# Kernel tuning notes

Hardware: AMD Instinct MI355X
Metric: run time of the kernel (lower is better)

## Reference

```python
import jax, jax.numpy as jnp
import numpy as np

S, B, E, H = 2048, 4, 512, 8
HD = E // H


def setup_inputs() -> dict:
    key = jax.random.key(0)
    ks = jax.random.split(key, 5)
    scale = 1.0 / np.sqrt(E)
    return {
        "query": jax.random.normal(ks[0], (S, B, E), jnp.float32),
        "key": jax.random.normal(ks[1], (S, B, E), jnp.float32),
        "value": jax.random.normal(ks[2], (S, B, E), jnp.float32),
        "in_proj_weight": jax.random.normal(ks[3], (3 * E, E), jnp.float32) * scale,
        "in_proj_bias": jnp.zeros((3 * E,), jnp.float32),
        "out_proj_weight": jax.random.normal(ks[4], (E, E), jnp.float32) * scale,
        "out_proj_bias": jnp.zeros((E,), jnp.float32),
    }


def reference(query, key, value, in_proj_weight, in_proj_bias, out_proj_weight, out_proj_bias):
    tgt_len, bsz, embed_dim = query.shape
    src_len = key.shape[0]
    # Quirk of this module: first chunk (w_qk) projects BOTH q and k; third chunk projects v.
    w_qk = in_proj_weight[:embed_dim]
    w_v = in_proj_weight[2 * embed_dim:]
    b_qk = in_proj_bias[:embed_dim]
    b_v = in_proj_bias[2 * embed_dim:]
    q = query @ w_qk.T + b_qk          # [S, B, E]
    k = key @ w_qk.T + b_qk
    v = value @ w_v.T + b_v
    # (S, B, E) -> (B*H, S, HD)
    def split_heads(x, n):
        return x.reshape(n, bsz * H, HD).transpose(1, 0, 2)
    q = split_heads(q, tgt_len) / jnp.sqrt(jnp.asarray(HD, q.dtype))
    k = split_heads(k, src_len)
    v = split_heads(v, src_len)
    scores = jnp.einsum("bqd,bkd->bqk", q, k)          # [B*H, S, S] full score matrix
    attn = jax.nn.softmax(scores, axis=-1)
    out = jnp.einsum("bqk,bkd->bqd", attn, v)          # [B*H, S, HD]
    out = out.transpose(1, 0, 2).reshape(tgt_len * bsz, embed_dim)
    out = out @ out_proj_weight.T + out_proj_bias
    return out.reshape(tgt_len, bsz, embed_dim)
```

## Files before the change

### kernel.cpp

```cpp
#include <hip/hip_runtime.h>
#include <hip/hip_bf16.h>

typedef __attribute__((ext_vector_type(8))) short s16x8;
typedef __attribute__((ext_vector_type(4))) short s16x4;
typedef __attribute__((ext_vector_type(4))) float f32x4;

#if __has_builtin(__builtin_amdgcn_exp2f)
#define EXP2F(x) __builtin_amdgcn_exp2f(x)
#else
#define EXP2F(x) exp2f(x)
#endif

#define S_LEN 2048
#define EMB   512
#define MROWS 8192

__device__ __forceinline__ short f2bf(float f) {
    union { float f; unsigned u; } z; z.f = f;
    unsigned r = z.u + 0x7FFF + ((z.u >> 16) & 1);
    return (short)(r >> 16);
}
__device__ __forceinline__ short f2bf_fast(float f) {
    union { float f; unsigned u; } z; z.f = f;
    return (short)((z.u + 0x8000u) >> 16);
}
__device__ __forceinline__ int swzs(int s) { return s ^ ((s >> 3) & 7); }

__device__ __forceinline__ void barrier_fast() {
    asm volatile("s_waitcnt lgkmcnt(0)" ::: "memory");
    __builtin_amdgcn_s_barrier();
    __builtin_amdgcn_sched_barrier(0);
}

__global__ __launch_bounds__(256) void w_to_bf16(const float* __restrict__ W,
                                                 short* __restrict__ wb, int n)
{
    int i = (blockIdx.x * 256 + threadIdx.x) * 8;
    if (i < n) {
        f32x4 a = *(const f32x4*)(W + i);
        f32x4 b = *(const f32x4*)(W + i + 4);
        s16x8 o;
        o[0] = f2bf(a[0]); o[1] = f2bf(a[1]); o[2] = f2bf(a[2]); o[3] = f2bf(a[3]);
        o[4] = f2bf(b[0]); o[5] = f2bf(b[1]); o[6] = f2bf(b[2]); o[7] = f2bf(b[3]);
        *(s16x8*)(wb + i) = o;
    }
}

template<int AF32, int BF32>
__device__ __forceinline__ void gemm_mainloop(const void* __restrict__ Ag,
                                              const void* __restrict__ Bg,
                                              short* sA, short* sB,
                                              f32x4 acc[2][4], int K)
{
    const int tid  = threadIdx.x;
    const int lane = tid & 63;
    const int wv   = tid >> 6;
    const int lsw  = lane ^ ((lane >> 3) & 7);
    const int amt  = (wv >> 1) * 2;
    const int bnt  = (wv & 1) * 4;

    const int brow = tid >> 2, bqd = tid & 3;
    const int boff = swzs((brow >> 4) * 64 + bqd * 16 + (brow & 15)) * 8;
    const int frow = tid >> 3, ffc = tid & 7;
    const int foff = swzs((frow >> 4) * 64 + (ffc >> 1) * 16 + (frow & 15)) * 8
                   + (ffc & 1) * 4;

    f32x4 aF0[2], aF1[2], bF0[2], bF1[2];
    s16x8 aH0, aH1, bH0, bH1;

    auto loadA = [&](int kt, f32x4 fr[2], s16x8& hr) {
        if (AF32) {
            const float* g = (const float*)Ag + (size_t)frow * K + kt + ffc * 4;
            fr[0] = *(const f32x4*)g;
            fr[1] = *(const f32x4*)(g + (size_t)64 * K);
        } else {
            hr = *(const s16x8*)((const short*)Ag + (size_t)brow * K + kt + bqd * 8);
        }
    };
    auto loadB = [&](int kt, f32x4 fr[2], s16x8& hr) {
        if (BF32) {
            const float* g = (const float*)Bg + (size_t)frow * K + kt + ffc * 4;
            fr[0] = *(const f32x4*)g;
            fr[1] = *(const f32x4*)(g + (size_t)64 * K);
        } else {
            hr = *(const s16x8*)((const short*)Bg + (size_t)brow * K + kt + bqd * 8);
        }
    };
    auto commit = [&](short* s, f32x4 fr[2], s16x8& hr, int F32) {
        if (F32) {
#pragma unroll
            for (int p = 0; p < 2; ++p) {
                s16x4 o4;
                o4[0] = f2bf_fast(fr[p][0]); o4[1] = f2bf_fast(fr[p][1]);
                o4[2] = f2bf_fast(fr[p][2]); o4[3] = f2bf_fast(fr[p][3]);
                *(s16x4*)(s + foff + p * 2048) = o4;
            }
        } else {
            *(s16x8*)(s + boff) = hr;
        }
    };
    auto compute = [&](const short* sAc, const short* sBc) {
        s16x8 a[2], b[4];
#pragma unroll
        for (int i = 0; i < 2; ++i)
            a[i] = *(const s16x8*)(sAc + ((amt + i) * 64 + lsw) * 8);
#pragma unroll
        for (int j = 0; j < 4; ++j)
            b[j] = *(const s16x8*)(sBc + ((bnt + j) * 64 + lsw) * 8);
#pragma unroll
        for (int i = 0; i < 2; ++i)
#pragma unroll
            for (int j = 0; j < 4; ++j)
                acc[i][j] = __builtin_amdgcn_mfma_f32_16x16x32_bf16(a[i], b[j], acc[i][j], 0, 0, 0);
    };

    loadA(0, aF0, aH0);  loadB(0, bF0, bH0);
    loadA(32, aF1, aH1); loadB(32, bF1, bH1);
    commit(sA, aF0, aH0, AF32); commit(sB, bF0, bH0, BF32);
    barrier_fast();

    for (int kt = 0; kt < K; kt += 64) {
        const int k2 = (kt + 64 < K) ? kt + 64 : 0;
        loadA(k2, aF0, aH0); loadB(k2, bF0, bH0);
        compute(sA, sB);
        commit(sA + 4096, aF1, aH1, AF32); commit(sB + 4096, bF1, bH1, BF32);
        barrier_fast();
        const int k3 = (kt + 96 < K) ? kt + 96 : 0;
        loadA(k3, aF1, aH1); loadB(k3, bF1, bH1);
        compute(sA + 4096, sB + 4096);
        commit(sA, aF0, aH0, AF32); commit(sB, bF0, bH0, BF32);
        barrier_fast();
    }
}

__global__ __launch_bounds__(512, 4) void qkv_proj(const float* __restrict__ query,
                                                   const float* __restrict__ key,
                                                   const float* __restrict__ value,
                                                   const short* __restrict__ wb,
                                                   const float* __restrict__ bias,
                                                   short* __restrict__ q,
                                                   short* __restrict__ k,
                                                   short* __restrict__ vt)
{
    __shared__ __align__(16) short smem[16384];
    short* sA = smem;
    short* sB = smem + 8192;

    const int z = blockIdx.z;
    const float* X  = (z == 0) ? query : (z == 1) ? key : value;
    const short* Wz = wb   + (z == 2 ? (size_t)1024 * EMB : 0);
    const float* bz = bias + (z == 2 ? 1024 : 0);
    const float scale = (z == 0) ? 0.125f * 1.44269504f : 1.0f;

    const int blockM = blockIdx.x * 128, blockN = blockIdx.y * 128;

    f32x4 acc[2][4];
#pragma unroll
    for (int i = 0; i < 2; ++i)
#pragma unroll
        for (int j = 0; j < 4; ++j)
            acc[i][j] = (f32x4){0.f, 0.f, 0.f, 0.f};

    gemm_mainloop<1, 0>(X + (size_t)blockM * EMB, Wz + (size_t)blockN * EMB,
                        sA, sB, acc, EMB);

    const int tid = threadIdx.x, lane = tid & 63, wv = tid >> 6;
    const int l15 = lane & 15, quad = lane >> 4;
    const int wm = (wv >> 1) * 32, wn = (wv & 1) * 64;

#pragma unroll
    for (int j = 0; j < 4; ++j) {
        int colL = wn + j * 16 + l15;
        float bval = bz[blockN + colL];
        int hL = colL >> 6, hd = colL & 63;
#pragma unroll
        for (int i = 0; i < 2; ++i) {
#pragma unroll
            for (int r = 0; r < 4; ++r) {
                int rowL = wm + i * 16 + quad * 4 + r;
                int b = rowL & 3, sp = rowL >> 2;
                float val = (acc[i][j][r] + bval) * scale;
                int idx;
                if (z == 2) {
                    int R = (b * 2 + hL) * 64 + hd;
                    idx = R * 32 + (((sp >> 3) ^ (R & 3)) << 3) + (sp & 7);
                } else {
                    idx = ((b * 2 + hL) * 32 + sp) * 64 + hd;
                }
                smem[idx] = f2bf(val);
            }
        }
    }
    barrier_fast();

    if (z == 2) {
        int R = tid;
        int b = tid >> 7, hL = (tid >> 6) & 1, hd = tid & 63;
        int h = (blockN >> 6) + hL;
        short* dst = vt + ((size_t)(b * 8 + h) * 64 + hd) * 2048 + (blockM >> 2);
#pragma unroll
        for (int u = 0; u < 4; ++u)
            ((s16x8*)dst)[u] = *(const s16x8*)(smem + R * 32 + ((u ^ (R & 3)) << 3));
    } else {
        const s16x8* src = (const s16x8*)(smem + tid * 32);
        int b = tid >> 7, hL = (tid >> 6) & 1;
        int sp = (tid >> 1) & 31, hdh = (tid & 1) * 32;
        int h = (blockN >> 6) + hL;
        short* dstp = (z == 0) ? q : k;
        short* dst = dstp + ((size_t)(b * 8 + h) * 2048 + (blockM >> 2) + sp) * 64 + hdh;
#pragma unroll
        for (int u = 0; u < 4; ++u) ((s16x8*)dst)[u] = src[u];
    }
}

__global__ __launch_bounds__(256, 2) void flash_attn(const short* __restrict__ q,
                                                     const short* __restrict__ k,
                                                     const short* __restrict__ vt,
                                                     short* __restrict__ attn)
{
    __shared__ __align__(16) short sK[2][4096];
    __shared__ __align__(16) short sV[2][4096];
    const int bh = blockIdx.x;
    const int q0 = blockIdx.y * 128;
    const int tid = threadIdx.x, wv = tid >> 6, lane = tid & 63;
    const int l15 = lane & 15, quad = lane >> 4;
    const int lsw = lane ^ ((lane >> 3) & 7);

    s16x8 qf[2][2];
#pragma unroll
    for (int qr = 0; qr < 2; ++qr) {
        const short* qp = q + ((size_t)(bh * 2048 + q0 + wv * 32 + qr * 16 + l15)) * 64 + quad * 8;
        qf[qr][0] = *(const s16x8*)qp;
        qf[qr][1] = *(const s16x8*)(qp + 32);
    }

    const short* kg = k  + (size_t)bh * 2048 * 64;
    const short* vg = vt + (size_t)bh * 64 * 2048;

    const int rk = tid >> 2, qd = tid & 3;
    const int pr = (rk & 35) | ((rk & 24) >> 1) | ((rk & 4) << 2);
    const int kw0 = swzs((pr >> 4) * 64 + qd * 16 + (pr & 15)) * 8;
    const int vw0 = swzs((rk >> 4) * 64 + qd * 16 + (rk & 15)) * 8;
    const short* kgt = kg + (size_t)rk * 64 + qd * 8;
    const short* vgt = vg + (size_t)rk * 2048 + qd * 8;

    f32x4 o[2][4];
    float ls[2][4];
#pragma unroll
    for (int qr = 0; qr < 2; ++qr)
#pragma unroll
        for (int i = 0; i < 4; ++i) { o[qr][i] = (f32x4){0.f, 0.f, 0.f, 0.f}; ls[qr][i] = 0.f; }

    s16x8 ka0, kb0, va0, vb0, ka1, kb1, va1, vb1;
    auto loadF = [&](int kt, s16x8& ka, s16x8& kb, s16x8& va, s16x8& vb) {
        ka = *(const s16x8*)(kgt + (size_t)kt * 64);
        kb = *(const s16x8*)(kgt + (size_t)kt * 64 + 32);
        va = *(const s16x8*)(vgt + kt);
        vb = *(const s16x8*)(vgt + kt + 32);
    };
    auto commitF = [&](short* Kb, short* Vb, s16x8& ka, s16x8& kb, s16x8& va, s16x8& vb) {
        *(s16x8*)(Kb + kw0)        = ka;
        *(s16x8*)(Kb + kw0 + 2048) = kb;
        *(s16x8*)(Vb + vw0)        = va;
        *(s16x8*)(Vb + vw0 + 2048) = vb;
    };
    auto computeT = [&](const short* Kc, const short* Vc) {
        f32x4 sc[2][4];
#pragma unroll
        for (int ct = 0; ct < 4; ++ct) {
            s16x8 kf0 = *(const s16x8*)(Kc + (ct * 64 + lsw) * 8);
            s16x8 kf1 = *(const s16x8*)(Kc + (ct * 64 + lsw) * 8 + 2048);
#pragma unroll
            for (int qr = 0; qr < 2; ++qr) {
                f32x4 c = (f32x4){0.f, 0.f, 0.f, 0.f};
                c = __builtin_amdgcn_mfma_f32_16x16x32_bf16(kf0, qf[qr][0], c, 0, 0, 0);
                c = __builtin_amdgcn_mfma_f32_16x16x32_bf16(kf1, qf[qr][1], c, 0, 0, 0);
                sc[qr][ct] = c;
            }
        }
        s16x8 pf[2][2];
#pragma unroll
        for (int qr = 0; qr < 2; ++qr)
#pragma unroll
            for (int c = 0; c < 2; ++c)
#pragma unroll
                for (int h = 0; h < 2; ++h)
#pragma unroll
                    for (int r = 0; r < 4; ++r) {
                        float p = EXP2F(sc[qr][2 * c + h][r]);
                        ls[qr][r] += p;
                        pf[qr][c][h * 4 + r] = f2bf_fast(p);
                    }
#pragma unroll
        for (int nt = 0; nt < 4; ++nt)
#pragma unroll
            for (int c = 0; c < 2; ++c) {
                s16x8 vf = *(const s16x8*)(Vc + ((c * 4 + nt) * 64 + lsw) * 8);
#pragma unroll
                for (int qr = 0; qr < 2; ++qr)
                    o[qr][nt] = __builtin_amdgcn_mfma_f32_16x16x32_bf16(pf[qr][c], vf, o[qr][nt], 0, 0, 0);
            }
    };

    loadF(0, ka0, kb0, va0, vb0);
    loadF(64, ka1, kb1, va1, vb1);
    commitF(sK[0], sV[0], ka0, kb0, va0, vb0);
    barrier_fast();

    for (int kt = 0; kt < 2048; kt += 128) {
        loadF((kt + 128) & 2047, ka0, kb0, va0, vb0);
        computeT(sK[0], sV[0]);
        commitF(sK[1], sV[1], ka1, kb1, va1, vb1);
        barrier_fast();
        loadF((kt + 192) & 2047, ka1, kb1, va1, vb1);
        computeT(sK[1], sV[1]);
        commitF(sK[0], sV[0], ka0, kb0, va0, vb0);
        barrier_fast();
    }

    const int b = bh >> 3, h = bh & 7;
#pragma unroll
    for (int qr = 0; qr < 2; ++qr) {
        float s = ls[qr][0] + ls[qr][1] + ls[qr][2] + ls[qr][3];
        s += __shfl_xor(s, 16, 64);
        s += __shfl_xor(s, 32, 64);
        float sinv = 1.0f / s;
        float inv[4];
#pragma unroll
        for (int r = 0; r < 4; ++r)
            inv[r] = __shfl(sinv, quad * 20 + r, 64);
#pragma unroll
        for (int r = 0; r < 4; ++r) {
            int srow = q0 + wv * 32 + qr * 16 + quad * 4 + r;
#pragma unroll
            for (int nt = 0; nt < 4; ++nt)
                attn[(size_t)(srow * 4 + b) * 512 + h * 64 + nt * 16 + l15] = f2bf(o[qr][nt][r] * inv[r]);
        }
    }
}

__global__ __launch_bounds__(512, 4) void out_proj(const short* __restrict__ attn,
                                                   const float* __restrict__ W,
                                                   const float* __restrict__ bias,
                                                   float* __restrict__ out)
{
    __shared__ __align__(16) short sA[2 * 4096], sB[2 * 4096];
    const int blockM = blockIdx.x * 128, blockN = blockIdx.y * 128;

    f32x4 acc[2][4];
#pragma unroll
    for (int i = 0; i < 2; ++i)
#pragma unroll
        for (int j = 0; j < 4; ++j)
            acc[i][j] = (f32x4){0.f, 0.f, 0.f, 0.f};

    gemm_mainloop<0, 1>(attn + (size_t)blockM * EMB, W + (size_t)blockN * EMB,
                        sA, sB, acc, EMB);

    const int tid = threadIdx.x, lane = tid & 63, wv = tid >> 6;
    const int l15 = lane & 15, quad = lane >> 4;
    const int wm = (wv >> 1) * 32, wn = (wv & 1) * 64;

#pragma unroll
    for (int j = 0; j < 4; ++j) {
        int col = blockN + wn + j * 16 + l15;
        float bval = bias[col];
#pragma unroll
        for (int i = 0; i < 2; ++i) {
#pragma unroll
            for (int r = 0; r < 4; ++r) {
                int row = blockM + wm + i * 16 + quad * 4 + r;
                out[(size_t)row * 512 + col] = acc[i][j][r] + bval;
            }
        }
    }
}

extern "C" void kernel_launch(void* const* d_in, const int* in_sizes, int n_in,
                              void* d_out, int out_size, void* d_ws, size_t ws_size,
                              hipStream_t stream)
{
    const float* query = (const float*)d_in[0];
    const float* key   = (const float*)d_in[1];
    const float* value = (const float*)d_in[2];
    const float* ipw   = (const float*)d_in[3];
    const float* ipb   = (const float*)d_in[4];
    const float* opw   = (const float*)d_in[5];
    const float* opb   = (const float*)d_in[6];
    float* out = (float*)d_out;

    const size_t NELEM = (size_t)MROWS * EMB;
    short* q    = (short*)d_ws;
    short* k    = q + NELEM;
    short* attn = k + NELEM;
    short* vt   = (short*)d_out;
    short* wb   = (short*)d_out + NELEM;

    w_to_bf16 <<<dim3(384),      256, 0, stream>>>(ipw, wb, 1536 * EMB);
    qkv_proj  <<<dim3(64, 4, 3), 512, 0, stream>>>(query, key, value, wb, ipb, q, k, vt);
    flash_attn<<<dim3(32, 16),   256, 0, stream>>>(q, k, vt, attn);
    out_proj  <<<dim3(64, 4),    512, 0, stream>>>(attn, opw, opb, out);
}
```

Baseline: 179.7 us.

## Double K/V tile to 128 keys per stage and interleave QK and PV phases

The flash attention loop now stages 128 keys per shared buffer instead of 64, halving the number of barriers per key sweep. Both 64-key QK products are issued before either softmax/PV phase so MFMA work can overlap with exp and LDS reads. This doubles LDS use (64KB per block) and register pressure from holding two score tiles and double the prefetch registers, which may reduce occupancy below the two blocks per CU the launch bounds request. The custom barrier is also replaced by __syncthreads.

New measurement: 181.3 us. No clear change (+0.9%).

```diff
diff --git a/kernel.cpp b/kernel.cpp
--- a/kernel.cpp
+++ b/kernel.cpp
@@ -218,8 +218,8 @@
                                                      const short* __restrict__ vt,
                                                      short* __restrict__ attn)
 {
-    __shared__ __align__(16) short sK[2][4096];
-    __shared__ __align__(16) short sV[2][4096];
+    __shared__ __align__(16) short sK[2][8192];
+    __shared__ __align__(16) short sV[2][8192];
     const int bh = blockIdx.x;
     const int q0 = blockIdx.y * 128;
     const int tid = threadIdx.x, wv = tid >> 6, lane = tid & 63;
@@ -251,21 +251,26 @@
 #pragma unroll
         for (int i = 0; i < 4; ++i) { o[qr][i] = (f32x4){0.f, 0.f, 0.f, 0.f}; ls[qr][i] = 0.f; }
 
-    s16x8 ka0, kb0, va0, vb0, ka1, kb1, va1, vb1;
-    auto loadF = [&](int kt, s16x8& ka, s16x8& kb, s16x8& va, s16x8& vb) {
-        ka = *(const s16x8*)(kgt + (size_t)kt * 64);
-        kb = *(const s16x8*)(kgt + (size_t)kt * 64 + 32);
-        va = *(const s16x8*)(vgt + kt);
-        vb = *(const s16x8*)(vgt + kt + 32);
-    };
-    auto commitF = [&](short* Kb, short* Vb, s16x8& ka, s16x8& kb, s16x8& va, s16x8& vb) {
-        *(s16x8*)(Kb + kw0)        = ka;
-        *(s16x8*)(Kb + kw0 + 2048) = kb;
-        *(s16x8*)(Vb + vw0)        = va;
-        *(s16x8*)(Vb + vw0 + 2048) = vb;
-    };
-    auto computeT = [&](const short* Kc, const short* Vc) {
-        f32x4 sc[2][4];
+    s16x8 kr[2][2], vr[2][2];
+    auto loadT = [&](int kt) {
+#pragma unroll
+        for (int s = 0; s < 2; ++s) {
+            kr[s][0] = *(const s16x8*)(kgt + (size_t)(kt + s * 64) * 64);
+            kr[s][1] = *(const s16x8*)(kgt + (size_t)(kt + s * 64) * 64 + 32);
+            vr[s][0] = *(const s16x8*)(vgt + kt + s * 64);
+            vr[s][1] = *(const s16x8*)(vgt + kt + s * 64 + 32);
+        }
+    };
+    auto commitT = [&](int buf) {
+#pragma unroll
+        for (int s = 0; s < 2; ++s) {
+            *(s16x8*)(sK[buf] + s * 4096 + kw0)        = kr[s][0];
+            *(s16x8*)(sK[buf] + s * 4096 + kw0 + 2048) = kr[s][1];
+            *(s16x8*)(sV[buf] + s * 4096 + vw0)        = vr[s][0];
+            *(s16x8*)(sV[buf] + s * 4096 + vw0 + 2048) = vr[s][1];
+        }
+    };
+    auto computeQK = [&](const short* Kc, f32x4 sc[2][4]) {
 #pragma unroll
         for (int ct = 0; ct < 4; ++ct) {
             s16x8 kf0 = *(const s16x8*)(Kc + (ct * 64 + lsw) * 8);
@@ -278,6 +283,8 @@
                 sc[qr][ct] = c;
             }
         }
+    };
+    auto softmaxPV = [&](f32x4 sc[2][4], const short* Vc) {
         s16x8 pf[2][2];
 #pragma unroll
         for (int qr = 0; qr < 2; ++qr)
@@ -302,20 +309,23 @@
             }
     };
 
-    loadF(0, ka0, kb0, va0, vb0);
-    loadF(64, ka1, kb1, va1, vb1);
-    commitF(sK[0], sV[0], ka0, kb0, va0, vb0);
-    barrier_fast();
-
+    loadT(0);
+    commitT(0);
+    __syncthreads();
+
+    int cur = 0;
     for (int kt = 0; kt < 2048; kt += 128) {
-        loadF((kt + 128) & 2047, ka0, kb0, va0, vb0);
-        computeT(sK[0], sV[0]);
-        commitF(sK[1], sV[1], ka1, kb1, va1, vb1);
-        barrier_fast();
-        loadF((kt + 192) & 2047, ka1, kb1, va1, vb1);
-        computeT(sK[1], sV[1]);
-        commitF(sK[0], sV[0], ka0, kb0, va0, vb0);
-        barrier_fast();
+        loadT((kt + 128) & 2047);
+
+        f32x4 sc0[2][4], sc1[2][4];
+        computeQK(sK[cur], sc0);
+        computeQK(sK[cur] + 4096, sc1);
+        softmaxPV(sc0, sV[cur]);
+        softmaxPV(sc1, sV[cur] + 4096);
+
+        commitT(cur ^ 1);
+        __syncthreads();
+        cur ^= 1;
     }
 
     const int b = bh >> 3, h = bh & 7;
```
